# Kernel optimization log

Hardware: AMD Instinct MI355X
Metric: run time of the kernel (lower is better)

## Reference

```python
import jax, jax.numpy as jnp
import numpy as np

N, DX, DZ, DY, H = 8192, 64, 128, 16, 512


def setup_inputs() -> dict:
    key = jax.random.key(0)
    ks = jax.random.split(key, 8)
    s1 = 1.0 / np.sqrt(DX)
    s2 = 1.0 / np.sqrt(H)
    return {
        "z_pred": jax.random.normal(ks[0], (N, DZ), dtype=jnp.float32),
        "x_label": jax.random.normal(ks[1], (N, DX), dtype=jnp.float32),
        "y_label": jax.random.normal(ks[2], (N, DY), dtype=jnp.float32),
        "W1": jax.random.normal(ks[3], (DX, H), dtype=jnp.float32) * s1,
        "b1": jnp.zeros((H,), dtype=jnp.float32),
        "W2": jax.random.normal(ks[4], (H, DZ), dtype=jnp.float32) * s2,
        "b2": jnp.zeros((DZ,), dtype=jnp.float32),
        "A": jax.random.normal(ks[5], (DZ, DZ), dtype=jnp.float32) * (1.0 / np.sqrt(DZ)),
        "B": jax.random.normal(ks[6], (DZ, DY), dtype=jnp.float32) * (1.0 / np.sqrt(DY)),
    }


def reference(z_pred, x_label, y_label, W1, b1, W2, b2, A, B):
    # forward_mapper T: x (dx,) -> (dz,), 2-layer tanh MLP
    def T(x):
        return jnp.tanh(x @ W1 + b1) @ W2 + b2

    # diff_eq: per-sample nonlinear dynamics x_dot = tanh(x)
    x_dot = jnp.tanh(x_label)  # (N, dx)

    # per-sample Jacobian dT/dx: (N, dz, dx). Equivalent to the torch code's
    # full N x N batched Jacobian followed by the diagonal slice, but without
    # the O(N^2) waste.
    jac = jax.vmap(jax.jacrev(T))(x_label)  # (N, dz, dx)

    dtdx_mul_f = jnp.einsum("nzd,nd->nz", jac, x_dot)  # (N, dz)
    m_mul_t = z_pred @ A.T                              # (N, dz)
    k_mul_h = y_label @ B.T                             # (N, dz)

    pde = dtdx_mul_f - m_mul_t - k_mul_h                # (N, dz)
    loss_batch = jnp.linalg.norm(pde, axis=1)           # (N,)
    return jnp.mean(loss_batch)
```

## Files before the change

kernel.cpp:

```cpp
#include <hip/hip_runtime.h>
#include <math.h>

#define Nn   8192
#define DXc  64
#define DZc  128
#define DYc  16
#define Hc   512
#define KCp  672
#define SSTR 520

typedef short bf16x8 __attribute__((ext_vector_type(8)));
typedef float f32x4  __attribute__((ext_vector_type(4)));

__device__ __forceinline__ float fast_tanh(float x) {
    float e = __expf(2.0f * x);
    return 1.0f - 2.0f / (e + 1.0f);
}
__device__ __forceinline__ short f2bf(float f) {
    unsigned u = __float_as_uint(f);
    return (short)((u + 0x7FFFu + ((u >> 16) & 1u)) >> 16);
}
__device__ __forceinline__ bf16x8 pack8(float4 a, float4 b) {
    bf16x8 r;
    r[0]=f2bf(a.x); r[1]=f2bf(a.y); r[2]=f2bf(a.z); r[3]=f2bf(a.w);
    r[4]=f2bf(b.x); r[5]=f2bf(b.y); r[6]=f2bf(b.z); r[7]=f2bf(b.w);
    return r;
}

__global__ void prep_kernel(const float* __restrict__ W1,
                            const float* __restrict__ W2,
                            const float* __restrict__ A,
                            const float* __restrict__ Bm,
                            short* __restrict__ W1T,
                            short* __restrict__ WcT) {
    __shared__ float tile[64 * 129];
    const int blk = blockIdx.x, t = threadIdx.x;

    if (blk < 8) {
        const int jb = blk * 64;
#pragma unroll
        for (int p = 0; p < 16; p++) {
            int lin = p * 256 + t;
            int k = lin >> 6, jj = lin & 63;
            tile[jj * 65 + k] = W1[(size_t)k * Hc + jb + jj];
        }
        __syncthreads();
#pragma unroll
        for (int p = 0; p < 2; p++) {
            int jj = p * 32 + (t >> 3), k8 = (t & 7) * 8;
            bf16x8 v;
#pragma unroll
            for (int i = 0; i < 8; i++) v[i] = f2bf(tile[jj * 65 + k8 + i]);
            *(bf16x8*)(W1T + (size_t)(jb + jj) * DXc + k8) = v;
        }
    } else if (blk < 16) {
        const int kb = (blk - 8) * 64;
#pragma unroll
        for (int p = 0; p < 32; p++) {
            int lin = p * 256 + t;
            int kk = lin >> 7, z = lin & 127;
            tile[kk * 129 + z] = W2[(size_t)(kb + kk) * DZc + z];
        }
        __syncthreads();
#pragma unroll
        for (int p = 0; p < 4; p++) {
            int z = p * 32 + (t >> 3), k8 = (t & 7) * 8;
            bf16x8 v;
#pragma unroll
            for (int i = 0; i < 8; i++) v[i] = f2bf(tile[(k8 + i) * 129 + z]);
            *(bf16x8*)(WcT + (size_t)z * KCp + kb + k8) = v;
        }
    } else if (blk < 24) {
        int idx8 = (blk - 16) * 256 + t;
        int z = idx8 >> 4, c8 = (idx8 & 15) * 8;
        float4 a0 = *(const float4*)(A + (size_t)z * DZc + c8);
        float4 a1 = *(const float4*)(A + (size_t)z * DZc + c8 + 4);
        bf16x8 v;
        v[0]=f2bf(-a0.x); v[1]=f2bf(-a0.y); v[2]=f2bf(-a0.z); v[3]=f2bf(-a0.w);
        v[4]=f2bf(-a1.x); v[5]=f2bf(-a1.y); v[6]=f2bf(-a1.z); v[7]=f2bf(-a1.w);
        *(bf16x8*)(WcT + (size_t)z * KCp + Hc + c8) = v;
    } else {
#pragma unroll
        for (int p = 0; p < 2; p++) {
            int cid = p * 256 + t;
            int z = cid >> 2, c8 = (cid & 3) * 8;
            bf16x8 v = (bf16x8){0,0,0,0,0,0,0,0};
            if (c8 < DYc) {
                float4 b0 = *(const float4*)(Bm + (size_t)z * DYc + c8);
                float4 b1 = *(const float4*)(Bm + (size_t)z * DYc + c8 + 4);
                v[0]=f2bf(-b0.x); v[1]=f2bf(-b0.y); v[2]=f2bf(-b0.z); v[3]=f2bf(-b0.w);
                v[4]=f2bf(-b1.x); v[5]=f2bf(-b1.y); v[6]=f2bf(-b1.z); v[7]=f2bf(-b1.w);
            }
            *(bf16x8*)(WcT + (size_t)z * KCp + Hc + DZc + c8) = v;
        }
    }
}

#define MFMA16(a, b, c) __builtin_amdgcn_mfma_f32_16x16x32_bf16((a), (b), (c), 0, 0, 0)

__global__ __launch_bounds__(256, 2)
void pde_main(const float* __restrict__ z_pred,
              const float* __restrict__ x_label,
              const float* __restrict__ y_label,
              const float* __restrict__ b1,
              const short* __restrict__ W1T,
              const short* __restrict__ WcT,
              float* __restrict__ partial) {
    __shared__ __align__(16) short sS[16 * SSTR];
    __shared__ float rsum[16];

    const int tid  = threadIdx.x;
    const int w    = tid >> 6;
    const int lane = tid & 63;
    const int n16  = lane & 15;
    const int q    = lane >> 4;
    const int n0   = blockIdx.x * 16;

    if (tid < 16) rsum[tid] = 0.f;

    const float* xp = x_label + (size_t)(n0 + n16) * DXc + q * 8;
    float4 x0 = *(const float4*)xp,        x1 = *(const float4*)(xp + 4);
    float4 x2 = *(const float4*)(xp + 32), x3 = *(const float4*)(xp + 36);
    bf16x8 ax0 = pack8(x0, x1), ax1 = pack8(x2, x3);
    bf16x8 at0, at1;
    {
        float v[16] = {x0.x,x0.y,x0.z,x0.w, x1.x,x1.y,x1.z,x1.w,
                       x2.x,x2.y,x2.z,x2.w, x3.x,x3.y,x3.z,x3.w};
#pragma unroll
        for (int i = 0; i < 8; i++) { at0[i] = f2bf(fast_tanh(v[i])); at1[i] = f2bf(fast_tanh(v[8 + i])); }
    }

#pragma unroll
    for (int cc = 0; cc < 2; cc++) {
        const int jb = w * 128 + cc * 64;
#pragma unroll
        for (int t = 0; t < 4; t++) {
            const int jt = jb + t * 16;
            const short* bp = W1T + (size_t)(jt + n16) * DXc + q * 8;
            bf16x8 bw0 = *(const bf16x8*)bp;
            bf16x8 bw1 = *(const bf16x8*)(bp + 32);
            f32x4 h = (f32x4){0.f,0.f,0.f,0.f};
            f32x4 u = (f32x4){0.f,0.f,0.f,0.f};
            h = MFMA16(ax0, bw0, h);  h = MFMA16(ax1, bw1, h);
            u = MFMA16(at0, bw0, u);  u = MFMA16(at1, bw1, u);
            const float bj = b1[jt + n16];
#pragma unroll
            for (int reg = 0; reg < 4; reg++) {
                float tv = fast_tanh(h[reg] + bj);
                float s  = (1.f - tv * tv) * u[reg];
                sS[(q * 4 + reg) * SSTR + jt + n16] = f2bf(s);
            }
        }
    }

    const int z0r = w * 32;
    const short* wr0 = WcT + (size_t)(z0r + n16) * KCp;
    const short* wr1 = WcT + (size_t)(z0r + 16 + n16) * KCp;
    f32x4 acc0 = (f32x4){0.f,0.f,0.f,0.f};
    f32x4 acc1 = (f32x4){0.f,0.f,0.f,0.f};

    {
        const float* zp = z_pred + (size_t)(n0 + n16) * DZc + q * 8;
#pragma unroll
        for (int kc = 0; kc < 4; kc++) {
            float4 a0 = *(const float4*)(zp + kc * 32);
            float4 a1 = *(const float4*)(zp + kc * 32 + 4);
            bf16x8 az = pack8(a0, a1);
            bf16x8 b0 = *(const bf16x8*)(wr0 + Hc + kc * 32 + q * 8);
            bf16x8 b1f = *(const bf16x8*)(wr1 + Hc + kc * 32 + q * 8);
            acc0 = MFMA16(az, b0, acc0);
            acc1 = MFMA16(az, b1f, acc1);
        }
    }
    {
        bf16x8 ay = (bf16x8){0,0,0,0,0,0,0,0};
        if (q < 2) {
            const float* yp = y_label + (size_t)(n0 + n16) * DYc + q * 8;
            float4 y0 = *(const float4*)yp, y1 = *(const float4*)(yp + 4);
            ay = pack8(y0, y1);
        }
        bf16x8 b0 = *(const bf16x8*)(wr0 + Hc + DZc + q * 8);
        bf16x8 b1f = *(const bf16x8*)(wr1 + Hc + DZc + q * 8);
        acc0 = MFMA16(ay, b0, acc0);
        acc1 = MFMA16(ay, b1f, acc1);
    }

    __syncthreads();

#pragma unroll
    for (int kc = 0; kc < 16; kc++) {
        bf16x8 sa = *(const bf16x8*)(sS + n16 * SSTR + kc * 32 + q * 8);
        bf16x8 b0 = *(const bf16x8*)(wr0 + kc * 32 + q * 8);
        bf16x8 b1f = *(const bf16x8*)(wr1 + kc * 32 + q * 8);
        acc0 = MFMA16(sa, b0, acc0);
        acc1 = MFMA16(sa, b1f, acc1);
    }

    float ss[4];
#pragma unroll
    for (int reg = 0; reg < 4; reg++) {
        ss[reg] = fmaf(acc0[reg], acc0[reg], acc1[reg] * acc1[reg]);
        ss[reg] += __shfl_xor(ss[reg], 1);
        ss[reg] += __shfl_xor(ss[reg], 2);
        ss[reg] += __shfl_xor(ss[reg], 4);
        ss[reg] += __shfl_xor(ss[reg], 8);
    }
    if (n16 == 0) {
#pragma unroll
        for (int reg = 0; reg < 4; reg++) atomicAdd(&rsum[q * 4 + reg], ss[reg]);
    }
    __syncthreads();

    if (tid == 0) {
        float s = 0.f;
#pragma unroll
        for (int i = 0; i < 16; i++) s += sqrtf(rsum[i]);
        partial[blockIdx.x] = s;
    }
}

__global__ void reduce_kernel(const float* __restrict__ partial, float* __restrict__ out) {
    __shared__ float s4[4];
    int tid = threadIdx.x;
    float v = partial[tid] + partial[tid + 256];
#pragma unroll
    for (int off = 32; off >= 1; off >>= 1) v += __shfl_down(v, off);
    if ((tid & 63) == 0) s4[tid >> 6] = v;
    __syncthreads();
    if (tid == 0) out[0] = (s4[0] + s4[1] + s4[2] + s4[3]) * (1.0f / (float)Nn);
}

extern "C" void kernel_launch(void* const* d_in, const int* in_sizes, int n_in,
                              void* d_out, int out_size, void* d_ws, size_t ws_size,
                              hipStream_t stream) {
    const float* z_pred  = (const float*)d_in[0];
    const float* x_label = (const float*)d_in[1];
    const float* y_label = (const float*)d_in[2];
    const float* W1      = (const float*)d_in[3];
    const float* b1      = (const float*)d_in[4];
    const float* W2      = (const float*)d_in[5];
    const float* A       = (const float*)d_in[7];
    const float* Bm      = (const float*)d_in[8];

    short* W1T = (short*)d_ws;
    short* WcT = W1T + Hc * DXc;
    float* partial = (float*)(WcT + DZc * KCp);

    prep_kernel<<<25, 256, 0, stream>>>(W1, W2, A, Bm, W1T, WcT);
    pde_main<<<Nn / 16, 256, 0, stream>>>(z_pred, x_label, y_label, b1, W1T, WcT, partial);
    reduce_kernel<<<1, 256, 0, stream>>>(partial, (float*)d_out);
}
```

Before: 89.23 us.

## Pre-swizzle weights into MFMA fragment layout, use 8 waves, fuse final reduction

The prep kernel now stores W1 and the fused W2/A/B matrix in a per-lane MFMA fragment order, so each lane fetches its bf16x8 operand with one contiguous, fully coalesced load. The LDS tile for the intermediate s matrix gets the same layout so the A-operand reads are linear. The main kernel moves to 512 threads (8 waves), each wave computing one 16-column z tile, which halves per-wave accumulator work. The separate reduce kernel is replaced by a memset plus a per-block atomicAdd into the output, which makes the floating-point summation order nondeterministic.

```diff
diff --git a/kernel.cpp b/kernel.cpp
--- a/kernel.cpp
+++ b/kernel.cpp
@@ -6,8 +6,7 @@
 #define DZc  128
 #define DYc  16
 #define Hc   512
-#define KCp  672
-#define SSTR 520
+#define NKC  21
 
 typedef short bf16x8 __attribute__((ext_vector_type(8)));
 typedef float f32x4  __attribute__((ext_vector_type(4)));
@@ -31,8 +30,8 @@
                             const float* __restrict__ W2,
                             const float* __restrict__ A,
                             const float* __restrict__ Bm,
-                            short* __restrict__ W1T,
-                            short* __restrict__ WcT) {
+                            short* __restrict__ Wb,
+                            short* __restrict__ Wf) {
     __shared__ float tile[64 * 129];
     const int blk = blockIdx.x, t = threadIdx.x;
 
@@ -47,11 +46,15 @@
         __syncthreads();
 #pragma unroll
         for (int p = 0; p < 2; p++) {
-            int jj = p * 32 + (t >> 3), k8 = (t & 7) * 8;
+            int cid = p * 256 + t;
+            int lane = cid & 63, q = lane >> 4, n16 = lane & 15;
+            int kc2 = (cid >> 6) & 1, jt4 = cid >> 7;
+            int jl = jt4 * 16 + n16, k0 = kc2 * 32 + q * 8;
             bf16x8 v;
 #pragma unroll
-            for (int i = 0; i < 8; i++) v[i] = f2bf(tile[jj * 65 + k8 + i]);
-            *(bf16x8*)(W1T + (size_t)(jb + jj) * DXc + k8) = v;
+            for (int i = 0; i < 8; i++) v[i] = f2bf(tile[jl * 65 + k0 + i]);
+            int block = ((blk * 4 + jt4) * 2 + kc2);
+            *(bf16x8*)(Wb + (size_t)(block * 64 + lane) * 8) = v;
         }
     } else if (blk < 16) {
         const int kb = (blk - 8) * 64;
@@ -64,50 +67,60 @@
         __syncthreads();
 #pragma unroll
         for (int p = 0; p < 4; p++) {
-            int z = p * 32 + (t >> 3), k8 = (t & 7) * 8;
+            int cid = p * 256 + t;
+            int lane = cid & 63, q = lane >> 4, n16 = lane & 15;
+            int rest = cid >> 6;
+            int kc2 = rest & 1, zt = rest >> 1;
+            int z = zt * 16 + n16, k0l = kc2 * 32 + q * 8;
             bf16x8 v;
 #pragma unroll
-            for (int i = 0; i < 8; i++) v[i] = f2bf(tile[(k8 + i) * 129 + z]);
-            *(bf16x8*)(WcT + (size_t)z * KCp + kb + k8) = v;
+            for (int i = 0; i < 8; i++) v[i] = f2bf(tile[(k0l + i) * 129 + z]);
+            int kc = (kb >> 5) + kc2;
+            *(bf16x8*)(Wf + (size_t)((zt * NKC + kc) * 64 + lane) * 8) = v;
         }
     } else if (blk < 24) {
-        int idx8 = (blk - 16) * 256 + t;
-        int z = idx8 >> 4, c8 = (idx8 & 15) * 8;
-        float4 a0 = *(const float4*)(A + (size_t)z * DZc + c8);
-        float4 a1 = *(const float4*)(A + (size_t)z * DZc + c8 + 4);
+        int cid = (blk - 16) * 256 + t;
+        int lane = cid & 63, q = lane >> 4, n16 = lane & 15;
+        int rest = cid >> 6;
+        int kcl = rest & 3, zt = rest >> 2;
+        int z = zt * 16 + n16, c0 = kcl * 32 + q * 8;
+        float4 a0 = *(const float4*)(A + (size_t)z * DZc + c0);
+        float4 a1 = *(const float4*)(A + (size_t)z * DZc + c0 + 4);
         bf16x8 v;
         v[0]=f2bf(-a0.x); v[1]=f2bf(-a0.y); v[2]=f2bf(-a0.z); v[3]=f2bf(-a0.w);
         v[4]=f2bf(-a1.x); v[5]=f2bf(-a1.y); v[6]=f2bf(-a1.z); v[7]=f2bf(-a1.w);
-        *(bf16x8*)(WcT + (size_t)z * KCp + Hc + c8) = v;
+        *(bf16x8*)(Wf + (size_t)((zt * NKC + 16 + kcl) * 64 + lane) * 8) = v;
     } else {
 #pragma unroll
         for (int p = 0; p < 2; p++) {
             int cid = p * 256 + t;
-            int z = cid >> 2, c8 = (cid & 3) * 8;
+            int lane = cid & 63, q = lane >> 4, n16 = lane & 15;
+            int zt = cid >> 6;
+            int z = zt * 16 + n16;
             bf16x8 v = (bf16x8){0,0,0,0,0,0,0,0};
-            if (c8 < DYc) {
-                float4 b0 = *(const float4*)(Bm + (size_t)z * DYc + c8);
-                float4 b1 = *(const float4*)(Bm + (size_t)z * DYc + c8 + 4);
+            if (q < 2) {
+                float4 b0 = *(const float4*)(Bm + (size_t)z * DYc + q * 8);
+                float4 b1 = *(const float4*)(Bm + (size_t)z * DYc + q * 8 + 4);
                 v[0]=f2bf(-b0.x); v[1]=f2bf(-b0.y); v[2]=f2bf(-b0.z); v[3]=f2bf(-b0.w);
                 v[4]=f2bf(-b1.x); v[5]=f2bf(-b1.y); v[6]=f2bf(-b1.z); v[7]=f2bf(-b1.w);
             }
-            *(bf16x8*)(WcT + (size_t)z * KCp + Hc + DZc + c8) = v;
+            *(bf16x8*)(Wf + (size_t)((zt * NKC + 20) * 64 + lane) * 8) = v;
         }
     }
 }
 
 #define MFMA16(a, b, c) __builtin_amdgcn_mfma_f32_16x16x32_bf16((a), (b), (c), 0, 0, 0)
 
-__global__ __launch_bounds__(256, 2)
+__global__ __launch_bounds__(512, 4)
 void pde_main(const float* __restrict__ z_pred,
               const float* __restrict__ x_label,
               const float* __restrict__ y_label,
               const float* __restrict__ b1,
-              const short* __restrict__ W1T,
-              const short* __restrict__ WcT,
-              float* __restrict__ partial) {
-    __shared__ __align__(16) short sS[16 * SSTR];
-    __shared__ float rsum[16];
+              const short* __restrict__ Wb,
+              const short* __restrict__ Wf,
+              float* __restrict__ out) {
+    __shared__ __align__(16) short sS[16 * 512];
+    __shared__ float red[8][16];
 
     const int tid  = threadIdx.x;
     const int w    = tid >> 6;
@@ -115,8 +128,6 @@
     const int n16  = lane & 15;
     const int q    = lane >> 4;
     const int n0   = blockIdx.x * 16;
-
-    if (tid < 16) rsum[tid] = 0.f;
 
     const float* xp = x_label + (size_t)(n0 + n16) * DXc + q * 8;
     float4 x0 = *(const float4*)xp,        x1 = *(const float4*)(xp + 4);
@@ -131,103 +142,77 @@
     }
 
 #pragma unroll
-    for (int cc = 0; cc < 2; cc++) {
-        const int jb = w * 128 + cc * 64;
-#pragma unroll
-        for (int t = 0; t < 4; t++) {
-            const int jt = jb + t * 16;
-            const short* bp = W1T + (size_t)(jt + n16) * DXc + q * 8;
-            bf16x8 bw0 = *(const bf16x8*)bp;
-            bf16x8 bw1 = *(const bf16x8*)(bp + 32);
-            f32x4 h = (f32x4){0.f,0.f,0.f,0.f};
-            f32x4 u = (f32x4){0.f,0.f,0.f,0.f};
-            h = MFMA16(ax0, bw0, h);  h = MFMA16(ax1, bw1, h);
-            u = MFMA16(at0, bw0, u);  u = MFMA16(at1, bw1, u);
-            const float bj = b1[jt + n16];
-#pragma unroll
-            for (int reg = 0; reg < 4; reg++) {
-                float tv = fast_tanh(h[reg] + bj);
-                float s  = (1.f - tv * tv) * u[reg];
-                sS[(q * 4 + reg) * SSTR + jt + n16] = f2bf(s);
-            }
-        }
-    }
-
-    const int z0r = w * 32;
-    const short* wr0 = WcT + (size_t)(z0r + n16) * KCp;
-    const short* wr1 = WcT + (size_t)(z0r + 16 + n16) * KCp;
-    f32x4 acc0 = (f32x4){0.f,0.f,0.f,0.f};
-    f32x4 acc1 = (f32x4){0.f,0.f,0.f,0.f};
-
+    for (int t = 0; t < 4; t++) {
+        const int jt = 4 * w + t;
+        const short* bp = Wb + (size_t)(jt * 2 * 64 + lane) * 8;
+        bf16x8 bw0 = *(const bf16x8*)bp;
+        bf16x8 bw1 = *(const bf16x8*)(bp + 512);
+        f32x4 h = (f32x4){0.f,0.f,0.f,0.f};
+        f32x4 u = (f32x4){0.f,0.f,0.f,0.f};
+        h = MFMA16(ax0, bw0, h);  h = MFMA16(ax1, bw1, h);
+        u = MFMA16(at0, bw0, u);  u = MFMA16(at1, bw1, u);
+        const float bj = b1[jt * 16 + n16];
+        const int j = jt * 16 + n16;
+        const int sbase = (j >> 5) * 512 + ((j >> 3) & 3) * 128 + (j & 7);
+#pragma unroll
+        for (int reg = 0; reg < 4; reg++) {
+            float tv = fast_tanh(h[reg] + bj);
+            float s  = (1.f - tv * tv) * u[reg];
+            sS[sbase + (q * 4 + reg) * 8] = f2bf(s);
+        }
+    }
+
+    const short* wfb = Wf + (size_t)(w * NKC * 64 + lane) * 8;
+    f32x4 acc = (f32x4){0.f,0.f,0.f,0.f};
     {
         const float* zp = z_pred + (size_t)(n0 + n16) * DZc + q * 8;
 #pragma unroll
-        for (int kc = 0; kc < 4; kc++) {
-            float4 a0 = *(const float4*)(zp + kc * 32);
-            float4 a1 = *(const float4*)(zp + kc * 32 + 4);
+        for (int kcl = 0; kcl < 4; kcl++) {
+            float4 a0 = *(const float4*)(zp + kcl * 32);
+            float4 a1 = *(const float4*)(zp + kcl * 32 + 4);
             bf16x8 az = pack8(a0, a1);
-            bf16x8 b0 = *(const bf16x8*)(wr0 + Hc + kc * 32 + q * 8);
-            bf16x8 b1f = *(const bf16x8*)(wr1 + Hc + kc * 32 + q * 8);
-            acc0 = MFMA16(az, b0, acc0);
-            acc1 = MFMA16(az, b1f, acc1);
-        }
-    }
-    {
+            bf16x8 bz = *(const bf16x8*)(wfb + (16 + kcl) * 512);
+            acc = MFMA16(az, bz, acc);
+        }
         bf16x8 ay = (bf16x8){0,0,0,0,0,0,0,0};
         if (q < 2) {
             const float* yp = y_label + (size_t)(n0 + n16) * DYc + q * 8;
-            float4 y0 = *(const float4*)yp, y1 = *(const float4*)(yp + 4);
-            ay = pack8(y0, y1);
-        }
-        bf16x8 b0 = *(const bf16x8*)(wr0 + Hc + DZc + q * 8);
-        bf16x8 b1f = *(const bf16x8*)(wr1 + Hc + DZc + q * 8);
-        acc0 = MFMA16(ay, b0, acc0);
-        acc1 = MFMA16(ay, b1f, acc1);
+            ay = pack8(*(const float4*)yp, *(const float4*)(yp + 4));
+        }
+        acc = MFMA16(ay, *(const bf16x8*)(wfb + 20 * 512), acc);
     }
 
     __syncthreads();
 
 #pragma unroll
     for (int kc = 0; kc < 16; kc++) {
-        bf16x8 sa = *(const bf16x8*)(sS + n16 * SSTR + kc * 32 + q * 8);
-        bf16x8 b0 = *(const bf16x8*)(wr0 + kc * 32 + q * 8);
-        bf16x8 b1f = *(const bf16x8*)(wr1 + kc * 32 + q * 8);
-        acc0 = MFMA16(sa, b0, acc0);
-        acc1 = MFMA16(sa, b1f, acc1);
-    }
-
-    float ss[4];
+        bf16x8 sa = *(const bf16x8*)(sS + kc * 512 + lane * 8);
+        bf16x8 bk = *(const bf16x8*)(wfb + kc * 512);
+        acc = MFMA16(sa, bk, acc);
+    }
+
 #pragma unroll
     for (int reg = 0; reg < 4; reg++) {
-        ss[reg] = fmaf(acc0[reg], acc0[reg], acc1[reg] * acc1[reg]);
-        ss[reg] += __shfl_xor(ss[reg], 1);
-        ss[reg] += __shfl_xor(ss[reg], 2);
-        ss[reg] += __shfl_xor(ss[reg], 4);
-        ss[reg] += __shfl_xor(ss[reg], 8);
-    }
-    if (n16 == 0) {
-#pragma unroll
-        for (int reg = 0; reg < 4; reg++) atomicAdd(&rsum[q * 4 + reg], ss[reg]);
+        float sq = acc[reg] * acc[reg];
+        sq += __shfl_xor(sq, 1);
+        sq += __shfl_xor(sq, 2);
+        sq += __shfl_xor(sq, 4);
+        sq += __shfl_xor(sq, 8);
+        if (n16 == 0) red[w][q * 4 + reg] = sq;
     }
     __syncthreads();
 
-    if (tid == 0) {
-        float s = 0.f;
-#pragma unroll
-        for (int i = 0; i < 16; i++) s += sqrtf(rsum[i]);
-        partial[blockIdx.x] = s;
-    }
-}
-
-__global__ void reduce_kernel(const float* __restrict__ partial, float* __restrict__ out) {
-    __shared__ float s4[4];
-    int tid = threadIdx.x;
-    float v = partial[tid] + partial[tid + 256];
-#pragma unroll
-    for (int off = 32; off >= 1; off >>= 1) v += __shfl_down(v, off);
-    if ((tid & 63) == 0) s4[tid >> 6] = v;
-    __syncthreads();
-    if (tid == 0) out[0] = (s4[0] + s4[1] + s4[2] + s4[3]) * (1.0f / (float)Nn);
+    if (tid < 16) {
+        float tot = 0.f;
+#pragma unroll
+        for (int i = 0; i < 8; i++) tot += red[i][tid];
+        float nrm = sqrtf(tot);
+        nrm += __shfl_xor(nrm, 1);
+        nrm += __shfl_xor(nrm, 2);
+        nrm += __shfl_xor(nrm, 4);
+        nrm += __shfl_xor(nrm, 8);
+        if (tid == 0) atomicAdd(out, nrm * (1.0f / (float)Nn));
+    }
 }
 
 extern "C" void kernel_launch(void* const* d_in, const int* in_sizes, int n_in,
@@ -242,11 +227,10 @@
     const float* A       = (const float*)d_in[7];
     const float* Bm      = (const float*)d_in[8];
 
-    short* W1T = (short*)d_ws;
-    short* WcT = W1T + Hc * DXc;
-    float* partial = (float*)(WcT + DZc * KCp);
-
-    prep_kernel<<<25, 256, 0, stream>>>(W1, W2, A, Bm, W1T, WcT);
-    pde_main<<<Nn / 16, 256, 0, stream>>>(z_pred, x_label, y_label, b1, W1T, WcT, partial);
-    reduce_kernel<<<1, 256, 0, stream>>>(partial, (float*)d_out);
-}
+    short* Wb = (short*)d_ws;
+    short* Wf = Wb + 512 * DXc;
+
+    hipMemsetAsync(d_out, 0, sizeof(float), stream);
+    prep_kernel<<<25, 256, 0, stream>>>(W1, W2, A, Bm, Wb, Wf);
+    pde_main<<<Nn / 16, 512, 0, stream>>>(z_pred, x_label, y_label, b1, Wb, Wf, (float*)d_out);
+}
```

Measured after the change: 95.44 us. +7.0%, slower.
